# Optimization experiments

Measured on AMD Instinct MI355X. Metric: run time of the kernel, lower is better.

The kernel has to match this reference:

```python
import jax, jax.numpy as jnp
import numpy as np

N_EMBED = 1024
HIDDEN = int(2 / 3 * 4 * N_EMBED)  # 2730, matches SwiGLU default
NUM_EXPERTS = 8
TOP_K = 2


def setup_inputs() -> dict:
    key = jax.random.key(0)
    ks = jax.random.split(key, 5)
    B, T, C, E, H = 2, 2048, N_EMBED, NUM_EXPERTS, HIDDEN
    s = 0.02
    return {
        "x": jax.random.normal(ks[0], (B, T, C), dtype=jnp.float32),
        "gate_w": jax.random.normal(ks[1], (E, C), dtype=jnp.float32) * s,  # Linear(C->E) weight [out,in]
        "w1": jax.random.normal(ks[2], (E, H, C), dtype=jnp.float32) * s,   # per-expert Linear(C->H)
        "w2": jax.random.normal(ks[3], (E, H, C), dtype=jnp.float32) * s,   # per-expert Linear(C->H)
        "w3": jax.random.normal(ks[4], (E, C, H), dtype=jnp.float32) * s,   # per-expert Linear(H->C)
    }


def reference(x, gate_w, w1, w2, w3):
    B, T, C = x.shape
    E = gate_w.shape[0]
    xt = x.reshape(-1, C)                      # [N, C], N = B*T
    N = xt.shape[0]

    # Router: top-k logits, softmax over the selected logits only
    logits = jnp.einsum("nc,ec->ne", xt, gate_w)          # [N, E]
    top_vals, top_idx = jax.lax.top_k(logits, TOP_K)       # [N, K]
    top_w = jax.nn.softmax(top_vals.astype(jnp.float32), axis=-1).astype(x.dtype)

    # Dense routing-weight matrix [N, E] (top-k indices are distinct per token)
    route = jnp.zeros((N, E), dtype=x.dtype)
    route = route.at[jnp.arange(N)[:, None], top_idx].set(top_w)

    # SwiGLU for all experts, batched over the expert axis (faithful math,
    # vectorized instead of the per-expert Python-loop gather/scatter)
    h1 = jnp.einsum("nc,ehc->enh", xt, w1)                 # [E, N, H]
    h2 = jnp.einsum("nc,ehc->enh", xt, w2)                 # [E, N, H]
    act = jax.nn.silu(h1) * h2                              # [E, N, H]
    expert_out = jnp.einsum("enh,ech->enc", act, w3)       # [E, N, C]

    out = jnp.einsum("ne,enc->nc", route, expert_out)      # weighted combine
    return out.reshape(B, T, C)
```

## Files before the change

### kernel.cpp

```cpp
#include <hip/hip_runtime.h>
#include <hip/hip_bf16.h>
#include <cstdint>
#include <cstddef>

#define TOKENS 4096
#define CDIM   1024
#define HDIM   2730
#define HPAD2  2816
#define NEXP   8
#define NPAIR  (TOKENS * 2)
#define NTB1   (HPAD2 / 128)
#define NTB2   (CDIM / 128)
#define NT1    (CDIM / 64)
#define NT2    (HPAD2 / 64)

typedef __bf16 bf16_t;
typedef bf16_t bf16x8 __attribute__((ext_vector_type(8)));
typedef float  f32x4  __attribute__((ext_vector_type(4)));

static __device__ __forceinline__ unsigned short f2bf(float f) {
    union { float f; unsigned int u; } v; v.f = f;
    unsigned int u = v.u;
    return (unsigned short)((u + 0x7FFFu + ((u >> 16) & 1u)) >> 16);
}
static __device__ __forceinline__ unsigned int pack2(float a, float b) {
    return (unsigned int)f2bf(a) | ((unsigned int)f2bf(b) << 16);
}

typedef __attribute__((address_space(3))) unsigned int lds_uint;
typedef const __attribute__((address_space(1))) unsigned int glob_uint;
static __device__ __forceinline__ void gl_lds16(const void* g, void* l) {
    __builtin_amdgcn_global_load_lds((glob_uint*)g, (lds_uint*)l, 16, 0, 0);
}


__global__ void moe_init(int* meta) {
    if (threadIdx.x < 64) meta[threadIdx.x] = 0;
}

__global__ __launch_bounds__(256) void moe_router(
    const float* __restrict__ x, const float* __restrict__ gw,
    int* __restrict__ meta, int* __restrict__ tok_idx, float* __restrict__ tok_w)
{
    int wave = threadIdx.x >> 6;
    int lane = threadIdx.x & 63;
    int t = blockIdx.x * 4 + wave;

    float acc[NEXP];
#pragma unroll
    for (int e = 0; e < NEXP; ++e) acc[e] = 0.f;

    const float4* xr = (const float4*)(x + (size_t)t * CDIM);
#pragma unroll
    for (int it = 0; it < 4; ++it) {
        int c4 = it * 64 + lane;
        float4 xv = xr[c4];
#pragma unroll
        for (int e = 0; e < NEXP; ++e) {
            float4 gv = ((const float4*)(gw + e * CDIM))[c4];
            acc[e] += xv.x * gv.x + xv.y * gv.y + xv.z * gv.z + xv.w * gv.w;
        }
    }
#pragma unroll
    for (int e = 0; e < NEXP; ++e) {
#pragma unroll
        for (int off = 32; off > 0; off >>= 1)
            acc[e] += __shfl_xor(acc[e], off, 64);
    }
    if (lane == 0) {
        int e0 = 0; float v0 = acc[0];
#pragma unroll
        for (int e = 1; e < NEXP; ++e) if (acc[e] > v0) { v0 = acc[e]; e0 = e; }
        int e1 = -1; float v1 = -3.0e38f;
#pragma unroll
        for (int e = 0; e < NEXP; ++e) if (e != e0 && acc[e] > v1) { v1 = acc[e]; e1 = e; }
        float w0 = 1.f / (1.f + __expf(v1 - v0));
        tok_idx[2 * t] = e0; tok_idx[2 * t + 1] = e1;
        tok_w[2 * t] = w0;  tok_w[2 * t + 1] = 1.f - w0;
        atomicAdd(&meta[e0], 1);
        atomicAdd(&meta[e1], 1);
    }
}

__global__ void moe_scan(int* meta) {
    if (threadIdx.x == 0) {
        int s = 0;
        for (int e = 0; e < NEXP; ++e) { meta[8 + e] = s; s += meta[e]; }
        meta[16] = s;
        int nb1 = 0;
        for (int e = 0; e < NEXP; ++e) {
            int beg = meta[8 + e], end = meta[8 + e] + meta[e];
            for (int m0 = beg; m0 < end; m0 += 256) {
                meta[32 + 2 * nb1] = e;
                meta[33 + 2 * nb1] = m0;
                ++nb1;
            }
        }
        meta[17] = nb1;
        int nb2 = 0;
        for (int e = 0; e < NEXP; ++e) {
            int beg = meta[8 + e], end = meta[8 + e] + meta[e];
            for (int m0 = beg; m0 < end; m0 += 128) {
                meta[128 + 2 * nb2] = e;
                meta[129 + 2 * nb2] = m0;
                ++nb2;
            }
        }
        meta[20] = nb2;
    }
}

__global__ __launch_bounds__(256) void moe_scatter(
    const int* __restrict__ tok_idx, const float* __restrict__ tok_w, int* meta,
    int* __restrict__ pair_token, float* __restrict__ pair_w)
{
    int t = blockIdx.x * 256 + threadIdx.x;
    if (t >= TOKENS) return;
#pragma unroll
    for (int k = 0; k < 2; ++k) {
        int e = tok_idx[2 * t + k];
        int pos = atomicAdd(&meta[24 + e], 1);
        int slot = meta[8 + e] + pos;
        pair_token[slot] = t;
        pair_w[slot] = tok_w[2 * t + k];
    }
}

__global__ __launch_bounds__(256) void moe_gather(
    const float* __restrict__ x, const int* __restrict__ pair_token,
    unsigned short* __restrict__ Xg)
{
    int base = blockIdx.x * 8;
    int i = threadIdx.x;
#pragma unroll
    for (int r = 0; r < 8; ++r) {
        int row = base + r;
        int t = pair_token[row];
        float4 v = ((const float4*)(x + (size_t)t * CDIM))[i];
        ushort4 o;
        o.x = f2bf(v.x); o.y = f2bf(v.y); o.z = f2bf(v.z); o.w = f2bf(v.w);
        ((ushort4*)(Xg + (size_t)row * CDIM))[i] = o;
    }
}

__global__ __launch_bounds__(256) void conv_w12(
    const float* __restrict__ w1, const float* __restrict__ w2,
    unsigned short* __restrict__ w1b, unsigned short* __restrict__ w2b)
{
    int e = blockIdx.y;
    const float* wsrc = blockIdx.z ? w2 : w1;
    unsigned short* wdst = blockIdx.z ? w2b : w1b;
    int col = threadIdx.x * 4;
#pragma unroll
    for (int r = 0; r < 8; ++r) {
        int row = blockIdx.x * 8 + r;
        unsigned short* dst = wdst + ((size_t)e * HPAD2 + row) * CDIM;
        uint2 pv;
        if (row < HDIM) {
            float4 a = *(const float4*)(wsrc + ((size_t)e * HDIM + row) * CDIM + col);
            pv.x = pack2(a.x, a.y); pv.y = pack2(a.z, a.w);
        } else {
            pv = uint2{0, 0};
        }
        *(uint2*)(dst + col) = pv;
    }
}

__global__ __launch_bounds__(256) void conv_w3(
    const float* __restrict__ w3, unsigned short* __restrict__ w3b)
{
    int e = blockIdx.y;
#pragma unroll
    for (int r = 0; r < 8; ++r) {
        int row = blockIdx.x * 8 + r;
        const float* src = w3 + ((size_t)e * CDIM + row) * HDIM;
        unsigned short* dst = w3b + ((size_t)e * CDIM + row) * HPAD2;
        for (int ch = threadIdx.x; ch < HPAD2 / 8; ch += 256) {
            int h = ch * 8;
            uint4 pv;
            if (h + 8 <= HDIM) {
                float2 a = *(const float2*)(src + h);
                float2 b = *(const float2*)(src + h + 2);
                float2 c = *(const float2*)(src + h + 4);
                float2 d = *(const float2*)(src + h + 6);
                pv.x = pack2(a.x, a.y); pv.y = pack2(b.x, b.y);
                pv.z = pack2(c.x, c.y); pv.w = pack2(d.x, d.y);
            } else if (h < HDIM) {
                float v[8];
#pragma unroll
                for (int q = 0; q < 8; ++q) v[q] = (h + q < HDIM) ? src[h + q] : 0.f;
                pv.x = pack2(v[0], v[1]); pv.y = pack2(v[2], v[3]);
                pv.z = pack2(v[4], v[5]); pv.w = pack2(v[6], v[7]);
            } else {
                pv = uint4{0, 0, 0, 0};
            }
            *(uint4*)(dst + h) = pv;
        }
    }
}

#define SWZ(row, ch) (((row) << 6) + ((((ch) ^ ((row) & 7))) << 3))

__global__ __launch_bounds__(512, 2) void moe_gemm1(
    const unsigned short* __restrict__ Xg,
    const unsigned short* __restrict__ w1b, const unsigned short* __restrict__ w2b,
    const float* __restrict__ pair_w, int* __restrict__ meta,
    unsigned short* __restrict__ act)
{
    __shared__ unsigned short sA[2][256 * 64];
    __shared__ unsigned short sB[2][256 * 64];
    __shared__ int sTile;

    int tid = threadIdx.x;
    int lane = tid & 63;
    int wv = tid >> 6;
    int wm = wv >> 2, wn = wv & 3;
    int l3 = lane >> 3;
    int srcc = (((lane & 7) ^ l3) << 3);

    int ntile = meta[17] * NTB1;

    for (;;) {
        if (tid == 0) sTile = atomicAdd(&meta[18], 1);
        __syncthreads();
        int t = sTile;
        if (t >= ntile) break;

        int bm = t / NTB1, bn = t - bm * NTB1;
        int e  = meta[32 + 2 * bm];
        int m0 = meta[33 + 2 * bm];
        int mEnd = meta[9 + e];
        int mEndm1 = mEnd - 1;
        int n0 = bn * 128;

        const unsigned short* w1e = w1b + (size_t)e * HPAD2 * CDIM + (size_t)n0 * CDIM;
        const unsigned short* w2e = w2b + (size_t)e * HPAD2 * CDIM + (size_t)n0 * CDIM;
        const unsigned short* bbase = (wv < 4) ? w1e : w2e;

        f32x4 acc1[8][2], acc2[8][2];
#pragma unroll
        for (int i = 0; i < 8; ++i)
#pragma unroll
            for (int j = 0; j < 2; ++j) {
                acc1[i][j] = {0.f, 0.f, 0.f, 0.f};
                acc2[i][j] = {0.f, 0.f, 0.f, 0.f};
            }

        auto STAGE = [&](int b, int kk) {
            int k0 = kk * 64;
#pragma unroll
            for (int i_ = 0; i_ < 4; ++i_) {
                int seg = wv * 4 + i_;
                int arow = seg * 8 + l3;
                int grow = m0 + arow; if (grow > mEndm1) grow = mEndm1;
                gl_lds16(Xg + (size_t)grow * CDIM + k0 + srcc, sA[b] + seg * 512);
                int bseg = (wv < 4) ? seg : seg - 16;
                gl_lds16(bbase + (size_t)(bseg * 8 + l3) * CDIM + k0 + srcc, sB[b] + seg * 512);
            }
        };

        STAGE(0, 0);
        __syncthreads();
        for (int t_ = 0; t_ < NT1; ++t_) {
            int cur = t_ & 1;
            if (t_ + 1 < NT1) STAGE(cur ^ 1, t_ + 1);
#pragma unroll
            for (int ks = 0; ks < 2; ++ks) {
                int kch = ks * 4 + (lane >> 4);
                bf16x8 af[8], b1f[2], b2f[2];
#pragma unroll
                for (int i = 0; i < 8; ++i) {
                    int r = wm * 128 + i * 16 + (lane & 15);
                    af[i] = *(const bf16x8*)(sA[cur] + SWZ(r, kch));
                }
#pragma unroll
                for (int j = 0; j < 2; ++j) {
                    int r1 = wn * 32 + j * 16 + (lane & 15);
                    b1f[j] = *(const bf16x8*)(sB[cur] + SWZ(r1, kch));
                    int r2 = 128 + r1;
                    b2f[j] = *(const bf16x8*)(sB[cur] + SWZ(r2, kch));
                }
#pragma unroll
                for (int i = 0; i < 8; ++i)
#pragma unroll
                    for (int j = 0; j < 2; ++j) {
                        acc1[i][j] = __builtin_amdgcn_mfma_f32_16x16x32_bf16(af[i], b1f[j], acc1[i][j], 0, 0, 0);
                        acc2[i][j] = __builtin_amdgcn_mfma_f32_16x16x32_bf16(af[i], b2f[j], acc2[i][j], 0, 0, 0);
                    }
            }
            __syncthreads();
        }

#pragma unroll
        for (int i = 0; i < 8; ++i) {
            int rbase = m0 + wm * 128 + i * 16 + ((lane >> 4) << 2);
#pragma unroll
            for (int r = 0; r < 4; ++r) {
                int grow = rbase + r;
                if (grow >= mEnd) continue;
                float pw = pair_w[grow];
                size_t rowoff = (size_t)grow * HPAD2;
#pragma unroll
                for (int j = 0; j < 2; ++j) {
                    int gcol = n0 + wn * 32 + j * 16 + (lane & 15);
                    float h1 = acc1[i][j][r], h2 = acc2[i][j][r];
                    float a = (h1 / (1.f + __expf(-h1))) * h2 * pw;
                    act[rowoff + gcol] = f2bf(a);
                }
            }
        }
    }
}

__global__ __launch_bounds__(512, 2) void moe_gemm2(
    const unsigned short* __restrict__ act,
    const unsigned short* __restrict__ w3b,
    int* __restrict__ meta, const int* __restrict__ pair_token,
    float* __restrict__ out)
{
    __shared__ unsigned short sA[2][128 * 64];
    __shared__ unsigned short sB[2][128 * 64];
    __shared__ int sTile;

    int tid = threadIdx.x;
    int lane = tid & 63;
    int wv = tid >> 6;
    int wm = wv >> 2, wn = wv & 3;
    int l3 = lane >> 3;
    int srcc = (((lane & 7) ^ l3) << 3);

    int ntile = meta[20] * NTB2;

    for (;;) {
        if (tid == 0) sTile = atomicAdd(&meta[19], 1);
        __syncthreads();
        int t = sTile;
        if (t >= ntile) break;

        int bm = t / NTB2, bn = t - bm * NTB2;
        int e  = meta[128 + 2 * bm];
        int m0 = meta[129 + 2 * bm];
        int mEnd = meta[9 + e];
        int mEndm1 = mEnd - 1;
        int n0 = bn * 128;

        const unsigned short* w3e = w3b + (size_t)e * CDIM * HPAD2 + (size_t)n0 * HPAD2;

        f32x4 acc[4][2];
#pragma unroll
        for (int i = 0; i < 4; ++i)
#pragma unroll
            for (int j = 0; j < 2; ++j) acc[i][j] = {0.f, 0.f, 0.f, 0.f};

        auto STAGE = [&](int b, int kk) {
            int k0 = kk * 64;
#pragma unroll
            for (int i_ = 0; i_ < 2; ++i_) {
                int seg = wv * 2 + i_;
                int row = seg * 8 + l3;
                int grow = m0 + row; if (grow > mEndm1) grow = mEndm1;
                gl_lds16(act + (size_t)grow * HPAD2 + k0 + srcc, sA[b] + seg * 512);
                gl_lds16(w3e + (size_t)row * HPAD2 + k0 + srcc, sB[b] + seg * 512);
            }
        };

        STAGE(0, 0);
        __syncthreads();
        for (int t_ = 0; t_ < NT2; ++t_) {
            int cur = t_ & 1;
            if (t_ + 1 < NT2) STAGE(cur ^ 1, t_ + 1);
#pragma unroll
            for (int ks = 0; ks < 2; ++ks) {
                int kch = ks * 4 + (lane >> 4);
                bf16x8 af[4], bf[2];
#pragma unroll
                for (int i = 0; i < 4; ++i) {
                    int r = wm * 64 + i * 16 + (lane & 15);
                    af[i] = *(const bf16x8*)(sA[cur] + SWZ(r, kch));
                }
#pragma unroll
                for (int j = 0; j < 2; ++j) {
                    int r = wn * 32 + j * 16 + (lane & 15);
                    bf[j] = *(const bf16x8*)(sB[cur] + SWZ(r, kch));
                }
#pragma unroll
                for (int i = 0; i < 4; ++i)
#pragma unroll
                    for (int j = 0; j < 2; ++j)
                        acc[i][j] = __builtin_amdgcn_mfma_f32_16x16x32_bf16(af[i], bf[j], acc[i][j], 0, 0, 0);
            }
            __syncthreads();
        }

#pragma unroll
        for (int i = 0; i < 4; ++i) {
            int rbase = m0 + wm * 64 + i * 16 + ((lane >> 4) << 2);
#pragma unroll
            for (int r = 0; r < 4; ++r) {
                int grow = rbase + r;
                if (grow >= mEnd) continue;
                int tok = pair_token[grow];
                float* orow = out + (size_t)tok * CDIM;
#pragma unroll
                for (int j = 0; j < 2; ++j) {
                    int gcol = n0 + wn * 32 + j * 16 + (lane & 15);
                    atomicAdd(orow + gcol, acc[i][j][r]);
                }
            }
        }
    }
}

extern "C" void kernel_launch(void* const* d_in, const int* in_sizes, int n_in,
                              void* d_out, int out_size, void* d_ws, size_t ws_size,
                              hipStream_t stream)
{
    const float* x  = (const float*)d_in[0];
    const float* gw = (const float*)d_in[1];
    const float* w1 = (const float*)d_in[2];
    const float* w2 = (const float*)d_in[3];
    const float* w3 = (const float*)d_in[4];
    float* out = (float*)d_out;

    char* ws = (char*)d_ws;
    size_t off = 0;
    auto alloc = [&](size_t bytes) -> void* {
        off = (off + 255) & ~(size_t)255;
        void* p = ws + off;
        off += bytes;
        return p;
    };
    int*   meta       = (int*)alloc(512 * sizeof(int));
    int*   tok_idx    = (int*)alloc((size_t)NPAIR * sizeof(int));
    float* tok_w      = (float*)alloc((size_t)NPAIR * sizeof(float));
    int*   pair_token = (int*)alloc((size_t)NPAIR * sizeof(int));
    float* pair_w     = (float*)alloc((size_t)NPAIR * sizeof(float));
    unsigned short* Xg  = (unsigned short*)alloc((size_t)NPAIR * CDIM * 2);
    unsigned short* act = (unsigned short*)alloc((size_t)NPAIR * HPAD2 * 2);
    unsigned short* w1b = (unsigned short*)alloc((size_t)NEXP * HPAD2 * CDIM * 2);
    unsigned short* w2b = (unsigned short*)alloc((size_t)NEXP * HPAD2 * CDIM * 2);
    unsigned short* w3b = (unsigned short*)alloc((size_t)NEXP * CDIM * HPAD2 * 2);
    (void)ws_size; (void)in_sizes; (void)n_in;

    hipMemsetAsync(d_out, 0, (size_t)out_size * sizeof(float), stream);

    moe_init<<<1, 64, 0, stream>>>(meta);
    moe_router<<<TOKENS / 4, 256, 0, stream>>>(x, gw, meta, tok_idx, tok_w);
    moe_scan<<<1, 64, 0, stream>>>(meta);
    moe_scatter<<<TOKENS / 256, 256, 0, stream>>>(tok_idx, tok_w, meta, pair_token, pair_w);
    moe_gather<<<NPAIR / 8, 256, 0, stream>>>(x, pair_token, Xg);
    conv_w12<<<dim3(HPAD2 / 8, NEXP, 2), 256, 0, stream>>>(w1, w2, w1b, w2b);
    conv_w3<<<dim3(CDIM / 8, NEXP), 256, 0, stream>>>(w3, w3b);
    moe_gemm1<<<256, 512, 0, stream>>>(Xg, w1b, w2b, pair_w, meta, act);
    moe_gemm2<<<512, 512, 0, stream>>>(act, w3b, meta, pair_token, out);
}
```

Before: 516.6 us.

## Split gemm2 K dimension in halves and combine per-pair outputs in separate kernel

gemm2 now splits the H reduction into two halves per output tile, doubling the tile count, and runs 256-thread blocks where each wave computes a 64x64 sub-tile instead of 64x32. Partial results are atomically added into a per-pair fp32 buffer indexed by slot, not scattered straight into the token output. A new combine kernel then sums each token's two expert rows, using a token-to-slot map recorded during scatter. This is meant to improve load balance and cut contention on token-row atomics. The cost is a larger memset, an extra 32MB buffer, and an additional combine pass.

```diff
diff --git a/kernel.cpp b/kernel.cpp
--- a/kernel.cpp
+++ b/kernel.cpp
@@ -12,7 +12,7 @@
 #define NTB1   (HPAD2 / 128)
 #define NTB2   (CDIM / 128)
 #define NT1    (CDIM / 64)
-#define NT2    (HPAD2 / 64)
+#define NT2H   (HPAD2 / 2 / 64)
 
 typedef __bf16 bf16_t;
 typedef bf16_t bf16x8 __attribute__((ext_vector_type(8)));
@@ -112,7 +112,7 @@
 
 __global__ __launch_bounds__(256) void moe_scatter(
     const int* __restrict__ tok_idx, const float* __restrict__ tok_w, int* meta,
-    int* __restrict__ pair_token, float* __restrict__ pair_w)
+    int* __restrict__ pair_token, float* __restrict__ pair_w, int* __restrict__ tok_slot)
 {
     int t = blockIdx.x * 256 + threadIdx.x;
     if (t >= TOKENS) return;
@@ -123,6 +123,7 @@
         int slot = meta[8 + e] + pos;
         pair_token[slot] = t;
         pair_w[slot] = tok_w[2 * t + k];
+        tok_slot[2 * t + k] = slot;
     }
 }
 
@@ -312,11 +313,11 @@
     }
 }
 
-__global__ __launch_bounds__(512, 2) void moe_gemm2(
+__global__ __launch_bounds__(256, 2) void moe_gemm2(
     const unsigned short* __restrict__ act,
     const unsigned short* __restrict__ w3b,
-    int* __restrict__ meta, const int* __restrict__ pair_token,
-    float* __restrict__ out)
+    int* __restrict__ meta,
+    float* __restrict__ pairout)
 {
     __shared__ unsigned short sA[2][128 * 64];
     __shared__ unsigned short sB[2][128 * 64];
@@ -325,11 +326,11 @@
     int tid = threadIdx.x;
     int lane = tid & 63;
     int wv = tid >> 6;
-    int wm = wv >> 2, wn = wv & 3;
+    int wm = wv >> 1, wn = wv & 1;
     int l3 = lane >> 3;
     int srcc = (((lane & 7) ^ l3) << 3);
 
-    int ntile = meta[20] * NTB2;
+    int ntile = meta[20] * NTB2 * 2;
 
     for (;;) {
         if (tid == 0) sTile = atomicAdd(&meta[19], 1);
@@ -337,26 +338,30 @@
         int t = sTile;
         if (t >= ntile) break;
 
-        int bm = t / NTB2, bn = t - bm * NTB2;
+        int bm = t >> 4;
+        int rem = t & 15;
+        int bn = rem >> 1;
+        int kh = rem & 1;
         int e  = meta[128 + 2 * bm];
         int m0 = meta[129 + 2 * bm];
         int mEnd = meta[9 + e];
         int mEndm1 = mEnd - 1;
         int n0 = bn * 128;
+        int kbase = kh * (HPAD2 / 2);
 
         const unsigned short* w3e = w3b + (size_t)e * CDIM * HPAD2 + (size_t)n0 * HPAD2;
 
-        f32x4 acc[4][2];
+        f32x4 acc[4][4];
 #pragma unroll
         for (int i = 0; i < 4; ++i)
 #pragma unroll
-            for (int j = 0; j < 2; ++j) acc[i][j] = {0.f, 0.f, 0.f, 0.f};
+            for (int j = 0; j < 4; ++j) acc[i][j] = {0.f, 0.f, 0.f, 0.f};
 
         auto STAGE = [&](int b, int kk) {
-            int k0 = kk * 64;
-#pragma unroll
-            for (int i_ = 0; i_ < 2; ++i_) {
-                int seg = wv * 2 + i_;
+            int k0 = kbase + kk * 64;
+#pragma unroll
+            for (int i_ = 0; i_ < 4; ++i_) {
+                int seg = wv * 4 + i_;
                 int row = seg * 8 + l3;
                 int grow = m0 + row; if (grow > mEndm1) grow = mEndm1;
                 gl_lds16(act + (size_t)grow * HPAD2 + k0 + srcc, sA[b] + seg * 512);
@@ -366,27 +371,27 @@
 
         STAGE(0, 0);
         __syncthreads();
-        for (int t_ = 0; t_ < NT2; ++t_) {
+        for (int t_ = 0; t_ < NT2H; ++t_) {
             int cur = t_ & 1;
-            if (t_ + 1 < NT2) STAGE(cur ^ 1, t_ + 1);
+            if (t_ + 1 < NT2H) STAGE(cur ^ 1, t_ + 1);
 #pragma unroll
             for (int ks = 0; ks < 2; ++ks) {
                 int kch = ks * 4 + (lane >> 4);
-                bf16x8 af[4], bf[2];
+                bf16x8 af[4], bf[4];
 #pragma unroll
                 for (int i = 0; i < 4; ++i) {
                     int r = wm * 64 + i * 16 + (lane & 15);
                     af[i] = *(const bf16x8*)(sA[cur] + SWZ(r, kch));
                 }
 #pragma unroll
-                for (int j = 0; j < 2; ++j) {
-                    int r = wn * 32 + j * 16 + (lane & 15);
+                for (int j = 0; j < 4; ++j) {
+                    int r = wn * 64 + j * 16 + (lane & 15);
                     bf[j] = *(const bf16x8*)(sB[cur] + SWZ(r, kch));
                 }
 #pragma unroll
                 for (int i = 0; i < 4; ++i)
 #pragma unroll
-                    for (int j = 0; j < 2; ++j)
+                    for (int j = 0; j < 4; ++j)
                         acc[i][j] = __builtin_amdgcn_mfma_f32_16x16x32_bf16(af[i], bf[j], acc[i][j], 0, 0, 0);
             }
             __syncthreads();
@@ -399,15 +404,32 @@
             for (int r = 0; r < 4; ++r) {
                 int grow = rbase + r;
                 if (grow >= mEnd) continue;
-                int tok = pair_token[grow];
-                float* orow = out + (size_t)tok * CDIM;
-#pragma unroll
-                for (int j = 0; j < 2; ++j) {
-                    int gcol = n0 + wn * 32 + j * 16 + (lane & 15);
+                float* orow = pairout + (size_t)grow * CDIM;
+#pragma unroll
+                for (int j = 0; j < 4; ++j) {
+                    int gcol = n0 + wn * 64 + j * 16 + (lane & 15);
                     atomicAdd(orow + gcol, acc[i][j][r]);
                 }
             }
         }
+    }
+}
+
+__global__ __launch_bounds__(256) void moe_combine(
+    const float* __restrict__ pairout, const int* __restrict__ tok_slot,
+    float* __restrict__ out)
+{
+    int base = blockIdx.x * 8;
+    int i = threadIdx.x;
+#pragma unroll
+    for (int r = 0; r < 8; ++r) {
+        int t = base + r;
+        int s0 = tok_slot[2 * t], s1 = tok_slot[2 * t + 1];
+        float4 a = ((const float4*)(pairout + (size_t)s0 * CDIM))[i];
+        float4 b = ((const float4*)(pairout + (size_t)s1 * CDIM))[i];
+        float4 o;
+        o.x = a.x + b.x; o.y = a.y + b.y; o.z = a.z + b.z; o.w = a.w + b.w;
+        ((float4*)(out + (size_t)t * CDIM))[i] = o;
     }
 }
 
@@ -433,24 +455,27 @@
     int*   meta       = (int*)alloc(512 * sizeof(int));
     int*   tok_idx    = (int*)alloc((size_t)NPAIR * sizeof(int));
     float* tok_w      = (float*)alloc((size_t)NPAIR * sizeof(float));
+    int*   tok_slot   = (int*)alloc((size_t)NPAIR * sizeof(int));
     int*   pair_token = (int*)alloc((size_t)NPAIR * sizeof(int));
     float* pair_w     = (float*)alloc((size_t)NPAIR * sizeof(float));
     unsigned short* Xg  = (unsigned short*)alloc((size_t)NPAIR * CDIM * 2);
     unsigned short* act = (unsigned short*)alloc((size_t)NPAIR * HPAD2 * 2);
+    float* pairout    = (float*)alloc((size_t)NPAIR * CDIM * sizeof(float));
     unsigned short* w1b = (unsigned short*)alloc((size_t)NEXP * HPAD2 * CDIM * 2);
     unsigned short* w2b = (unsigned short*)alloc((size_t)NEXP * HPAD2 * CDIM * 2);
     unsigned short* w3b = (unsigned short*)alloc((size_t)NEXP * CDIM * HPAD2 * 2);
-    (void)ws_size; (void)in_sizes; (void)n_in;
-
-    hipMemsetAsync(d_out, 0, (size_t)out_size * sizeof(float), stream);
+    (void)ws_size; (void)in_sizes; (void)n_in; (void)out_size;
+
+    hipMemsetAsync(pairout, 0, (size_t)NPAIR * CDIM * sizeof(float), stream);
 
     moe_init<<<1, 64, 0, stream>>>(meta);
     moe_router<<<TOKENS / 4, 256, 0, stream>>>(x, gw, meta, tok_idx, tok_w);
     moe_scan<<<1, 64, 0, stream>>>(meta);
-    moe_scatter<<<TOKENS / 256, 256, 0, stream>>>(tok_idx, tok_w, meta, pair_token, pair_w);
+    moe_scatter<<<TOKENS / 256, 256, 0, stream>>>(tok_idx, tok_w, meta, pair_token, pair_w, tok_slot);
     moe_gather<<<NPAIR / 8, 256, 0, stream>>>(x, pair_token, Xg);
     conv_w12<<<dim3(HPAD2 / 8, NEXP, 2), 256, 0, stream>>>(w1, w2, w1b, w2b);
     conv_w3<<<dim3(CDIM / 8, NEXP), 256, 0, stream>>>(w3, w3b);
     moe_gemm1<<<256, 512, 0, stream>>>(Xg, w1b, w2b, pair_w, meta, act);
-    moe_gemm2<<<512, 512, 0, stream>>>(act, w3b, meta, pair_token, out);
-}
+    moe_gemm2<<<512, 256, 0, stream>>>(act, w3b, meta, pairout);
+    moe_combine<<<TOKENS / 8, 256, 0, stream>>>(pairout, tok_slot, out);
+}
```

After: 548.1 us. +6.1%, slower.

## Restructure gemm1 main loop into four phased MFMA blocks with early prefetch

Applied to the files above, without the earlier changes.

The gate/up GEMM main loop is split into four sub-phases, each covering half of the M rows and either the w1 or w2 half. Each phase does its own LDS fragment loads and MFMA block, separated by raw s_barrier calls and s_setprio raising around the MFMAs. Global-to-LDS staging is split into separate A and B stages and issued two K-steps ahead into the buffer just consumed, with explicit vmcnt waits. The aim is to interleave LDS reads, global loads and MFMA so matrix work keeps flowing and register pressure drops, at the cost of many more barriers and fragile manual waitcnt accounting.

```diff
diff --git a/kernel.cpp b/kernel.cpp
--- a/kernel.cpp
+++ b/kernel.cpp
@@ -216,6 +216,7 @@
     int wv = tid >> 6;
     int wm = wv >> 2, wn = wv & 3;
     int l3 = lane >> 3;
+    int l15 = lane & 15, l4 = lane >> 4;
     int srcc = (((lane & 7) ^ l3) << 3);
 
     int ntile = meta[17] * NTB1;
@@ -246,7 +247,7 @@
                 acc2[i][j] = {0.f, 0.f, 0.f, 0.f};
             }
 
-        auto STAGE = [&](int b, int kk) {
+        auto STAGE_A = [&](int b, int kk) {
             int k0 = kk * 64;
 #pragma unroll
             for (int i_ = 0; i_ < 4; ++i_) {
@@ -254,46 +255,115 @@
                 int arow = seg * 8 + l3;
                 int grow = m0 + arow; if (grow > mEndm1) grow = mEndm1;
                 gl_lds16(Xg + (size_t)grow * CDIM + k0 + srcc, sA[b] + seg * 512);
+            }
+        };
+        auto STAGE_B = [&](int b, int kk) {
+            int k0 = kk * 64;
+#pragma unroll
+            for (int i_ = 0; i_ < 4; ++i_) {
+                int seg = wv * 4 + i_;
                 int bseg = (wv < 4) ? seg : seg - 16;
                 gl_lds16(bbase + (size_t)(bseg * 8 + l3) * CDIM + k0 + srcc, sB[b] + seg * 512);
             }
         };
 
-        STAGE(0, 0);
-        __syncthreads();
+        STAGE_A(0, 0); STAGE_B(0, 0);
+        STAGE_A(1, 1); STAGE_B(1, 1);
+        asm volatile("s_waitcnt vmcnt(8)" ::: "memory");
+        __builtin_amdgcn_s_barrier();
+
         for (int t_ = 0; t_ < NT1; ++t_) {
             int cur = t_ & 1;
-            if (t_ + 1 < NT1) STAGE(cur ^ 1, t_ + 1);
+            const unsigned short* A = sA[cur];
+            const unsigned short* B = sB[cur];
+            bf16x8 af[2][4], b1f[2][2], b2f[2][2];
+
 #pragma unroll
             for (int ks = 0; ks < 2; ++ks) {
-                int kch = ks * 4 + (lane >> 4);
-                bf16x8 af[8], b1f[2], b2f[2];
-#pragma unroll
-                for (int i = 0; i < 8; ++i) {
-                    int r = wm * 128 + i * 16 + (lane & 15);
-                    af[i] = *(const bf16x8*)(sA[cur] + SWZ(r, kch));
-                }
-#pragma unroll
-                for (int j = 0; j < 2; ++j) {
-                    int r1 = wn * 32 + j * 16 + (lane & 15);
-                    b1f[j] = *(const bf16x8*)(sB[cur] + SWZ(r1, kch));
-                    int r2 = 128 + r1;
-                    b2f[j] = *(const bf16x8*)(sB[cur] + SWZ(r2, kch));
-                }
-#pragma unroll
-                for (int i = 0; i < 8; ++i)
-#pragma unroll
-                    for (int j = 0; j < 2; ++j) {
-                        acc1[i][j] = __builtin_amdgcn_mfma_f32_16x16x32_bf16(af[i], b1f[j], acc1[i][j], 0, 0, 0);
-                        acc2[i][j] = __builtin_amdgcn_mfma_f32_16x16x32_bf16(af[i], b2f[j], acc2[i][j], 0, 0, 0);
-                    }
-            }
-            __syncthreads();
+                int kch = ks * 4 + l4;
+#pragma unroll
+                for (int i = 0; i < 4; ++i)
+                    af[ks][i] = *(const bf16x8*)(A + SWZ(wm * 128 + i * 16 + l15, kch));
+#pragma unroll
+                for (int j = 0; j < 2; ++j)
+                    b1f[ks][j] = *(const bf16x8*)(B + SWZ(wn * 32 + j * 16 + l15, kch));
+            }
+            __builtin_amdgcn_s_barrier();
+            asm volatile("s_waitcnt lgkmcnt(0)" ::: "memory");
+            __builtin_amdgcn_s_setprio(1);
+#pragma unroll
+            for (int ks = 0; ks < 2; ++ks)
+#pragma unroll
+                for (int i = 0; i < 4; ++i)
+#pragma unroll
+                    for (int j = 0; j < 2; ++j)
+                        acc1[i][j] = __builtin_amdgcn_mfma_f32_16x16x32_bf16(af[ks][i], b1f[ks][j], acc1[i][j], 0, 0, 0);
+            __builtin_amdgcn_s_setprio(0);
+            __builtin_amdgcn_s_barrier();
+
+#pragma unroll
+            for (int ks = 0; ks < 2; ++ks) {
+                int kch = ks * 4 + l4;
+#pragma unroll
+                for (int j = 0; j < 2; ++j)
+                    b2f[ks][j] = *(const bf16x8*)(B + SWZ(128 + wn * 32 + j * 16 + l15, kch));
+            }
+            __builtin_amdgcn_s_barrier();
+            asm volatile("s_waitcnt lgkmcnt(0)" ::: "memory");
+            __builtin_amdgcn_s_setprio(1);
+#pragma unroll
+            for (int ks = 0; ks < 2; ++ks)
+#pragma unroll
+                for (int i = 0; i < 4; ++i)
+#pragma unroll
+                    for (int j = 0; j < 2; ++j)
+                        acc2[i][j] = __builtin_amdgcn_mfma_f32_16x16x32_bf16(af[ks][i], b2f[ks][j], acc2[i][j], 0, 0, 0);
+            __builtin_amdgcn_s_setprio(0);
+            __builtin_amdgcn_s_barrier();
+
+#pragma unroll
+            for (int ks = 0; ks < 2; ++ks) {
+                int kch = ks * 4 + l4;
+#pragma unroll
+                for (int i = 0; i < 4; ++i)
+                    af[ks][i] = *(const bf16x8*)(A + SWZ(wm * 128 + 64 + i * 16 + l15, kch));
+            }
+            if (t_ + 2 < NT1) STAGE_B(cur, t_ + 2);
+            __builtin_amdgcn_s_barrier();
+            asm volatile("s_waitcnt lgkmcnt(0)" ::: "memory");
+            __builtin_amdgcn_s_setprio(1);
+#pragma unroll
+            for (int ks = 0; ks < 2; ++ks)
+#pragma unroll
+                for (int i = 0; i < 4; ++i)
+#pragma unroll
+                    for (int j = 0; j < 2; ++j)
+                        acc1[4 + i][j] = __builtin_amdgcn_mfma_f32_16x16x32_bf16(af[ks][i], b1f[ks][j], acc1[4 + i][j], 0, 0, 0);
+            __builtin_amdgcn_s_setprio(0);
+            __builtin_amdgcn_s_barrier();
+
+            if (t_ + 2 < NT1) {
+                STAGE_A(cur, t_ + 2);
+                asm volatile("s_waitcnt vmcnt(8)" ::: "memory");
+            } else {
+                asm volatile("s_waitcnt vmcnt(0)" ::: "memory");
+            }
+            __builtin_amdgcn_s_barrier();
+            __builtin_amdgcn_s_setprio(1);
+#pragma unroll
+            for (int ks = 0; ks < 2; ++ks)
+#pragma unroll
+                for (int i = 0; i < 4; ++i)
+#pragma unroll
+                    for (int j = 0; j < 2; ++j)
+                        acc2[4 + i][j] = __builtin_amdgcn_mfma_f32_16x16x32_bf16(af[ks][i], b2f[ks][j], acc2[4 + i][j], 0, 0, 0);
+            __builtin_amdgcn_s_setprio(0);
+            __builtin_amdgcn_s_barrier();
         }
 
 #pragma unroll
         for (int i = 0; i < 8; ++i) {
-            int rbase = m0 + wm * 128 + i * 16 + ((lane >> 4) << 2);
+            int rbase = m0 + wm * 128 + ((i & 3) * 16) + ((i >> 2) * 64) + (l4 << 2);
 #pragma unroll
             for (int r = 0; r < 4; ++r) {
                 int grow = rbase + r;
@@ -302,8 +372,9 @@
                 size_t rowoff = (size_t)grow * HPAD2;
 #pragma unroll
                 for (int j = 0; j < 2; ++j) {
-                    int gcol = n0 + wn * 32 + j * 16 + (lane & 15);
-                    float h1 = acc1[i][j][r], h2 = acc2[i][j][r];
+                    int gcol = n0 + wn * 32 + j * 16 + l15;
+                    int ai = (i & 3) + ((i >> 2) << 2);
+                    float h1 = acc1[ai][j][r], h2 = acc2[ai][j][r];
                     float a = (h1 / (1.f + __expf(-h1))) * h2 * pw;
                     act[rowoff + gcol] = f2bf(a);
                 }
```

Result: no change. 510.0 us (-1.3%).

## Fuse both expert GEMMs into one persistent kernel with per-row-block dependency counters

Applied to the files above, without the earlier changes.

Merges the gate/up GEMM and the down-projection GEMM into a single persistent kernel that pulls tiles from one shared queue: all GEMM1 tiles come first, then GEMM2 tiles. Each GEMM2 tile spins until the completion counter of its parent GEMM1 row block reaches the number of N tiles, signalled through threadfence and atomics. This removes the kernel boundary and the tail idle time between the two GEMMs, so GEMM2 work can overlap the end of GEMM1. In exchange it adds spin-wait latency and per-tile fences, and GEMM2 now runs with the larger LDS allocation, which may limit occupancy.

```diff
diff --git a/kernel.cpp b/kernel.cpp
--- a/kernel.cpp
+++ b/kernel.cpp
@@ -35,7 +35,7 @@
 
 
 __global__ void moe_init(int* meta) {
-    if (threadIdx.x < 64) meta[threadIdx.x] = 0;
+    meta[threadIdx.x] = 0;
 }
 
 __global__ __launch_bounds__(256) void moe_router(
@@ -87,26 +87,27 @@
         int s = 0;
         for (int e = 0; e < NEXP; ++e) { meta[8 + e] = s; s += meta[e]; }
         meta[16] = s;
-        int nb1 = 0;
+        int nb1 = 0, nb2 = 0;
         for (int e = 0; e < NEXP; ++e) {
             int beg = meta[8 + e], end = meta[8 + e] + meta[e];
+            int g1base = nb1;
             for (int m0 = beg; m0 < end; m0 += 256) {
                 meta[32 + 2 * nb1] = e;
                 meta[33 + 2 * nb1] = m0;
                 ++nb1;
             }
-        }
-        meta[17] = nb1;
-        int nb2 = 0;
-        for (int e = 0; e < NEXP; ++e) {
-            int beg = meta[8 + e], end = meta[8 + e] + meta[e];
+            int k2 = 0;
             for (int m0 = beg; m0 < end; m0 += 128) {
                 meta[128 + 2 * nb2] = e;
                 meta[129 + 2 * nb2] = m0;
-                ++nb2;
+                meta[320 + nb2] = g1base + (k2 >> 1);
+                ++k2; ++nb2;
             }
         }
+        meta[17] = nb1;
         meta[20] = nb2;
+        meta[21] = nb1 * NTB1;
+        meta[22] = nb1 * NTB1 + nb2 * NTB2;
     }
 }
 
@@ -201,11 +202,13 @@
 
 #define SWZ(row, ch) (((row) << 6) + ((((ch) ^ ((row) & 7))) << 3))
 
-__global__ __launch_bounds__(512, 2) void moe_gemm1(
+__global__ __launch_bounds__(512, 2) void moe_gemms(
     const unsigned short* __restrict__ Xg,
     const unsigned short* __restrict__ w1b, const unsigned short* __restrict__ w2b,
+    const unsigned short* __restrict__ w3b,
     const float* __restrict__ pair_w, int* __restrict__ meta,
-    unsigned short* __restrict__ act)
+    const int* __restrict__ pair_token,
+    unsigned short* __restrict__ act, float* __restrict__ out)
 {
     __shared__ unsigned short sA[2][256 * 64];
     __shared__ unsigned short sB[2][256 * 64];
@@ -214,200 +217,185 @@
     int tid = threadIdx.x;
     int lane = tid & 63;
     int wv = tid >> 6;
-    int wm = wv >> 2, wn = wv & 3;
     int l3 = lane >> 3;
+    int l15 = lane & 15, l4 = lane >> 4;
     int srcc = (((lane & 7) ^ l3) << 3);
 
-    int ntile = meta[17] * NTB1;
+    int ntile1 = meta[21];
+    int ntileT = meta[22];
 
     for (;;) {
         if (tid == 0) sTile = atomicAdd(&meta[18], 1);
         __syncthreads();
         int t = sTile;
-        if (t >= ntile) break;
-
-        int bm = t / NTB1, bn = t - bm * NTB1;
-        int e  = meta[32 + 2 * bm];
-        int m0 = meta[33 + 2 * bm];
-        int mEnd = meta[9 + e];
-        int mEndm1 = mEnd - 1;
-        int n0 = bn * 128;
-
-        const unsigned short* w1e = w1b + (size_t)e * HPAD2 * CDIM + (size_t)n0 * CDIM;
-        const unsigned short* w2e = w2b + (size_t)e * HPAD2 * CDIM + (size_t)n0 * CDIM;
-        const unsigned short* bbase = (wv < 4) ? w1e : w2e;
-
-        f32x4 acc1[8][2], acc2[8][2];
-#pragma unroll
-        for (int i = 0; i < 8; ++i)
-#pragma unroll
-            for (int j = 0; j < 2; ++j) {
-                acc1[i][j] = {0.f, 0.f, 0.f, 0.f};
-                acc2[i][j] = {0.f, 0.f, 0.f, 0.f};
-            }
-
-        auto STAGE = [&](int b, int kk) {
-            int k0 = kk * 64;
-#pragma unroll
-            for (int i_ = 0; i_ < 4; ++i_) {
-                int seg = wv * 4 + i_;
-                int arow = seg * 8 + l3;
-                int grow = m0 + arow; if (grow > mEndm1) grow = mEndm1;
-                gl_lds16(Xg + (size_t)grow * CDIM + k0 + srcc, sA[b] + seg * 512);
-                int bseg = (wv < 4) ? seg : seg - 16;
-                gl_lds16(bbase + (size_t)(bseg * 8 + l3) * CDIM + k0 + srcc, sB[b] + seg * 512);
-            }
-        };
-
-        STAGE(0, 0);
+        if (t >= ntileT) break;
+
+        if (t < ntile1) {
+            int bm = t / NTB1, bn = t - bm * NTB1;
+            int e  = meta[32 + 2 * bm];
+            int m0 = meta[33 + 2 * bm];
+            int mEnd = meta[9 + e];
+            int mEndm1 = mEnd - 1;
+            int n0 = bn * 128;
+            int wm = wv >> 2, wn = wv & 3;
+
+            const unsigned short* w1e = w1b + (size_t)e * HPAD2 * CDIM + (size_t)n0 * CDIM;
+            const unsigned short* w2e = w2b + (size_t)e * HPAD2 * CDIM + (size_t)n0 * CDIM;
+            const unsigned short* bbase = (wv < 4) ? w1e : w2e;
+
+            f32x4 acc1[8][2], acc2[8][2];
+#pragma unroll
+            for (int i = 0; i < 8; ++i)
+#pragma unroll
+                for (int j = 0; j < 2; ++j) {
+                    acc1[i][j] = {0.f, 0.f, 0.f, 0.f};
+                    acc2[i][j] = {0.f, 0.f, 0.f, 0.f};
+                }
+
+            auto STAGE = [&](int b, int kk) {
+                int k0 = kk * 64;
+#pragma unroll
+                for (int i_ = 0; i_ < 4; ++i_) {
+                    int seg = wv * 4 + i_;
+                    int arow = seg * 8 + l3;
+                    int grow = m0 + arow; if (grow > mEndm1) grow = mEndm1;
+                    gl_lds16(Xg + (size_t)grow * CDIM + k0 + srcc, sA[b] + seg * 512);
+                    int bseg = (wv < 4) ? seg : seg - 16;
+                    gl_lds16(bbase + (size_t)(bseg * 8 + l3) * CDIM + k0 + srcc, sB[b] + seg * 512);
+                }
+            };
+
+            STAGE(0, 0);
+            __syncthreads();
+            for (int t_ = 0; t_ < NT1; ++t_) {
+                int cur = t_ & 1;
+                if (t_ + 1 < NT1) STAGE(cur ^ 1, t_ + 1);
+#pragma unroll
+                for (int ks = 0; ks < 2; ++ks) {
+                    int kch = ks * 4 + l4;
+                    bf16x8 af[8], b1f[2], b2f[2];
+#pragma unroll
+                    for (int i = 0; i < 8; ++i)
+                        af[i] = *(const bf16x8*)(sA[cur] + SWZ(wm * 128 + i * 16 + l15, kch));
+#pragma unroll
+                    for (int j = 0; j < 2; ++j) {
+                        int r1 = wn * 32 + j * 16 + l15;
+                        b1f[j] = *(const bf16x8*)(sB[cur] + SWZ(r1, kch));
+                        b2f[j] = *(const bf16x8*)(sB[cur] + SWZ(128 + r1, kch));
+                    }
+#pragma unroll
+                    for (int i = 0; i < 8; ++i)
+#pragma unroll
+                        for (int j = 0; j < 2; ++j) {
+                            acc1[i][j] = __builtin_amdgcn_mfma_f32_16x16x32_bf16(af[i], b1f[j], acc1[i][j], 0, 0, 0);
+                            acc2[i][j] = __builtin_amdgcn_mfma_f32_16x16x32_bf16(af[i], b2f[j], acc2[i][j], 0, 0, 0);
+                        }
+                }
+                __syncthreads();
+            }
+
+#pragma unroll
+            for (int i = 0; i < 8; ++i) {
+                int rbase = m0 + wm * 128 + i * 16 + (l4 << 2);
+#pragma unroll
+                for (int r = 0; r < 4; ++r) {
+                    int grow = rbase + r;
+                    if (grow >= mEnd) continue;
+                    float pw = pair_w[grow];
+                    size_t rowoff = (size_t)grow * HPAD2;
+#pragma unroll
+                    for (int j = 0; j < 2; ++j) {
+                        int gcol = n0 + wn * 32 + j * 16 + l15;
+                        float h1 = acc1[i][j][r], h2 = acc2[i][j][r];
+                        float a = (h1 / (1.f + __expf(-h1))) * h2 * pw;
+                        act[rowoff + gcol] = f2bf(a);
+                    }
+                }
+            }
+            __threadfence();
+            __syncthreads();
+            if (tid == 0) atomicAdd(&meta[400 + bm], 1);
+        } else {
+            int t2 = t - ntile1;
+            int bm = t2 >> 3, bn = t2 & 7;
+            int parent = meta[320 + bm];
+            if (tid == 0) {
+                while (__hip_atomic_load(&meta[400 + parent], __ATOMIC_RELAXED,
+                                         __HIP_MEMORY_SCOPE_AGENT) < NTB1)
+                    __builtin_amdgcn_s_sleep(32);
+            }
+            __syncthreads();
+            __threadfence();
+
+            int e  = meta[128 + 2 * bm];
+            int m0 = meta[129 + 2 * bm];
+            int mEnd = meta[9 + e];
+            int mEndm1 = mEnd - 1;
+            int n0 = bn * 128;
+            int wm = wv >> 2, wn = wv & 3;
+
+            const unsigned short* w3e = w3b + (size_t)e * CDIM * HPAD2 + (size_t)n0 * HPAD2;
+
+            f32x4 acc[4][2];
+#pragma unroll
+            for (int i = 0; i < 4; ++i)
+#pragma unroll
+                for (int j = 0; j < 2; ++j) acc[i][j] = {0.f, 0.f, 0.f, 0.f};
+
+            auto STAGE2 = [&](int b, int kk) {
+                int k0 = kk * 64;
+#pragma unroll
+                for (int i_ = 0; i_ < 2; ++i_) {
+                    int seg = wv * 2 + i_;
+                    int row = seg * 8 + l3;
+                    int grow = m0 + row; if (grow > mEndm1) grow = mEndm1;
+                    gl_lds16(act + (size_t)grow * HPAD2 + k0 + srcc, sA[b] + seg * 512);
+                    gl_lds16(w3e + (size_t)row * HPAD2 + k0 + srcc, sB[b] + seg * 512);
+                }
+            };
+
+            STAGE2(0, 0);
+            __syncthreads();
+            for (int t_ = 0; t_ < NT2; ++t_) {
+                int cur = t_ & 1;
+                if (t_ + 1 < NT2) STAGE2(cur ^ 1, t_ + 1);
+#pragma unroll
+                for (int ks = 0; ks < 2; ++ks) {
+                    int kch = ks * 4 + l4;
+                    bf16x8 af[4], bf[2];
+#pragma unroll
+                    for (int i = 0; i < 4; ++i)
+                        af[i] = *(const bf16x8*)(sA[cur] + SWZ(wm * 64 + i * 16 + l15, kch));
+#pragma unroll
+                    for (int j = 0; j < 2; ++j)
+                        bf[j] = *(const bf16x8*)(sB[cur] + SWZ(wn * 32 + j * 16 + l15, kch));
+#pragma unroll
+                    for (int i = 0; i < 4; ++i)
+#pragma unroll
+                        for (int j = 0; j < 2; ++j)
+                            acc[i][j] = __builtin_amdgcn_mfma_f32_16x16x32_bf16(af[i], bf[j], acc[i][j], 0, 0, 0);
+                }
+                __syncthreads();
+            }
+
+#pragma unroll
+            for (int i = 0; i < 4; ++i) {
+                int rbase = m0 + wm * 64 + i * 16 + (l4 << 2);
+#pragma unroll
+                for (int r = 0; r < 4; ++r) {
+                    int grow = rbase + r;
+                    if (grow >= mEnd) continue;
+                    int tok = pair_token[grow];
+                    float* orow = out + (size_t)tok * CDIM;
+#pragma unroll
+                    for (int j = 0; j < 2; ++j) {
+                        int gcol = n0 + wn * 32 + j * 16 + l15;
+                        atomicAdd(orow + gcol, acc[i][j][r]);
+                    }
+                }
+            }
+        }
         __syncthreads();
-        for (int t_ = 0; t_ < NT1; ++t_) {
-            int cur = t_ & 1;
-            if (t_ + 1 < NT1) STAGE(cur ^ 1, t_ + 1);
-#pragma unroll
-            for (int ks = 0; ks < 2; ++ks) {
-                int kch = ks * 4 + (lane >> 4);
-                bf16x8 af[8], b1f[2], b2f[2];
-#pragma unroll
-                for (int i = 0; i < 8; ++i) {
-                    int r = wm * 128 + i * 16 + (lane & 15);
-                    af[i] = *(const bf16x8*)(sA[cur] + SWZ(r, kch));
-                }
-#pragma unroll
-                for (int j = 0; j < 2; ++j) {
-                    int r1 = wn * 32 + j * 16 + (lane & 15);
-                    b1f[j] = *(const bf16x8*)(sB[cur] + SWZ(r1, kch));
-                    int r2 = 128 + r1;
-                    b2f[j] = *(const bf16x8*)(sB[cur] + SWZ(r2, kch));
-                }
-#pragma unroll
-                for (int i = 0; i < 8; ++i)
-#pragma unroll
-                    for (int j = 0; j < 2; ++j) {
-                        acc1[i][j] = __builtin_amdgcn_mfma_f32_16x16x32_bf16(af[i], b1f[j], acc1[i][j], 0, 0, 0);
-                        acc2[i][j] = __builtin_amdgcn_mfma_f32_16x16x32_bf16(af[i], b2f[j], acc2[i][j], 0, 0, 0);
-                    }
-            }
-            __syncthreads();
-        }
-
-#pragma unroll
-        for (int i = 0; i < 8; ++i) {
-            int rbase = m0 + wm * 128 + i * 16 + ((lane >> 4) << 2);
-#pragma unroll
-            for (int r = 0; r < 4; ++r) {
-                int grow = rbase + r;
-                if (grow >= mEnd) continue;
-                float pw = pair_w[grow];
-                size_t rowoff = (size_t)grow * HPAD2;
-#pragma unroll
-                for (int j = 0; j < 2; ++j) {
-                    int gcol = n0 + wn * 32 + j * 16 + (lane & 15);
-                    float h1 = acc1[i][j][r], h2 = acc2[i][j][r];
-                    float a = (h1 / (1.f + __expf(-h1))) * h2 * pw;
-                    act[rowoff + gcol] = f2bf(a);
-                }
-            }
-        }
-    }
-}
-
-__global__ __launch_bounds__(512, 2) void moe_gemm2(
-    const unsigned short* __restrict__ act,
-    const unsigned short* __restrict__ w3b,
-    int* __restrict__ meta, const int* __restrict__ pair_token,
-    float* __restrict__ out)
-{
-    __shared__ unsigned short sA[2][128 * 64];
-    __shared__ unsigned short sB[2][128 * 64];
-    __shared__ int sTile;
-
-    int tid = threadIdx.x;
-    int lane = tid & 63;
-    int wv = tid >> 6;
-    int wm = wv >> 2, wn = wv & 3;
-    int l3 = lane >> 3;
-    int srcc = (((lane & 7) ^ l3) << 3);
-
-    int ntile = meta[20] * NTB2;
-
-    for (;;) {
-        if (tid == 0) sTile = atomicAdd(&meta[19], 1);
-        __syncthreads();
-        int t = sTile;
-        if (t >= ntile) break;
-
-        int bm = t / NTB2, bn = t - bm * NTB2;
-        int e  = meta[128 + 2 * bm];
-        int m0 = meta[129 + 2 * bm];
-        int mEnd = meta[9 + e];
-        int mEndm1 = mEnd - 1;
-        int n0 = bn * 128;
-
-        const unsigned short* w3e = w3b + (size_t)e * CDIM * HPAD2 + (size_t)n0 * HPAD2;
-
-        f32x4 acc[4][2];
-#pragma unroll
-        for (int i = 0; i < 4; ++i)
-#pragma unroll
-            for (int j = 0; j < 2; ++j) acc[i][j] = {0.f, 0.f, 0.f, 0.f};
-
-        auto STAGE = [&](int b, int kk) {
-            int k0 = kk * 64;
-#pragma unroll
-            for (int i_ = 0; i_ < 2; ++i_) {
-                int seg = wv * 2 + i_;
-                int row = seg * 8 + l3;
-                int grow = m0 + row; if (grow > mEndm1) grow = mEndm1;
-                gl_lds16(act + (size_t)grow * HPAD2 + k0 + srcc, sA[b] + seg * 512);
-                gl_lds16(w3e + (size_t)row * HPAD2 + k0 + srcc, sB[b] + seg * 512);
-            }
-        };
-
-        STAGE(0, 0);
-        __syncthreads();
-        for (int t_ = 0; t_ < NT2; ++t_) {
-            int cur = t_ & 1;
-            if (t_ + 1 < NT2) STAGE(cur ^ 1, t_ + 1);
-#pragma unroll
-            for (int ks = 0; ks < 2; ++ks) {
-                int kch = ks * 4 + (lane >> 4);
-                bf16x8 af[4], bf[2];
-#pragma unroll
-                for (int i = 0; i < 4; ++i) {
-                    int r = wm * 64 + i * 16 + (lane & 15);
-                    af[i] = *(const bf16x8*)(sA[cur] + SWZ(r, kch));
-                }
-#pragma unroll
-                for (int j = 0; j < 2; ++j) {
-                    int r = wn * 32 + j * 16 + (lane & 15);
-                    bf[j] = *(const bf16x8*)(sB[cur] + SWZ(r, kch));
-                }
-#pragma unroll
-                for (int i = 0; i < 4; ++i)
-#pragma unroll
-                    for (int j = 0; j < 2; ++j)
-                        acc[i][j] = __builtin_amdgcn_mfma_f32_16x16x32_bf16(af[i], bf[j], acc[i][j], 0, 0, 0);
-            }
-            __syncthreads();
-        }
-
-#pragma unroll
-        for (int i = 0; i < 4; ++i) {
-            int rbase = m0 + wm * 64 + i * 16 + ((lane >> 4) << 2);
-#pragma unroll
-            for (int r = 0; r < 4; ++r) {
-                int grow = rbase + r;
-                if (grow >= mEnd) continue;
-                int tok = pair_token[grow];
-                float* orow = out + (size_t)tok * CDIM;
-#pragma unroll
-                for (int j = 0; j < 2; ++j) {
-                    int gcol = n0 + wn * 32 + j * 16 + (lane & 15);
-                    atomicAdd(orow + gcol, acc[i][j][r]);
-                }
-            }
-        }
     }
 }
 
@@ -444,13 +432,12 @@
 
     hipMemsetAsync(d_out, 0, (size_t)out_size * sizeof(float), stream);
 
-    moe_init<<<1, 64, 0, stream>>>(meta);
+    moe_init<<<1, 512, 0, stream>>>(meta);
     moe_router<<<TOKENS / 4, 256, 0, stream>>>(x, gw, meta, tok_idx, tok_w);
     moe_scan<<<1, 64, 0, stream>>>(meta);
     moe_scatter<<<TOKENS / 256, 256, 0, stream>>>(tok_idx, tok_w, meta, pair_token, pair_w);
     moe_gather<<<NPAIR / 8, 256, 0, stream>>>(x, pair_token, Xg);
     conv_w12<<<dim3(HPAD2 / 8, NEXP, 2), 256, 0, stream>>>(w1, w2, w1b, w2b);
     conv_w3<<<dim3(CDIM / 8, NEXP), 256, 0, stream>>>(w3, w3b);
-    moe_gemm1<<<256, 512, 0, stream>>>(Xg, w1b, w2b, pair_w, meta, act);
-    moe_gemm2<<<512, 512, 0, stream>>>(act, w3b, meta, pair_token, out);
-}
+    moe_gemms<<<256, 512, 0, stream>>>(Xg, w1b, w2b, w3b, pair_w, meta, pair_token, act, out);
+}
```

New measurement: 837.7 us. 1.62x slower.
